# Kernel tuning notes

Hardware: AMD Instinct MI355X
Metric: run time of the kernel (lower is better)

## Reference

```python
import jax, jax.numpy as jnp
from jax import lax
import numpy as np

E = 16          # n_routed_experts
H = 2048        # hidden_size
I = 1408        # moe_intermediate_size
T = 2048        # tokens
K = 6           # top_k


def setup_inputs() -> dict:
    key = jax.random.key(0)
    k1, k2, k3, k4, k5 = jax.random.split(key, 5)
    hidden_states = jax.random.normal(k1, (T, H), dtype=jnp.float32)
    top_k_index = jax.random.randint(k2, (T, K), 0, E)
    top_k_weights = jax.random.uniform(k3, (T, K), dtype=jnp.float32)
    gate_up_proj = jax.random.normal(k4, (E, 2 * I, H), dtype=jnp.float32) * 0.02
    down_proj = jax.random.normal(k5, (E, H, I), dtype=jnp.float32) * 0.02
    return {
        "hidden_states": hidden_states,
        "top_k_index": top_k_index,
        "top_k_weights": top_k_weights,
        "gate_up_proj": gate_up_proj,
        "down_proj": down_proj,
    }


def reference(hidden_states, top_k_index, top_k_weights, gate_up_proj, down_proj):
    # combine[t, e] = sum over k-slots of top_k_weights[t, k] where top_k_index[t, k] == e
    # (scatter-add handles duplicate expert picks identically to index_add_).
    n_tok = hidden_states.shape[0]
    n_exp = gate_up_proj.shape[0]
    combine = jnp.zeros((n_tok, n_exp), hidden_states.dtype)
    combine = combine.at[jnp.arange(n_tok)[:, None], top_k_index].add(top_k_weights)

    def expert_step(acc, params):
        gu, dn, c_e = params  # gu: [2I, H], dn: [H, I], c_e: [n_tok]
        gate, up = jnp.split(hidden_states @ gu.T, 2, axis=-1)  # each [n_tok, I]
        y = (jax.nn.silu(gate) * up) @ dn.T                     # [n_tok, H]
        return acc + y * c_e[:, None], None

    out, _ = lax.scan(
        expert_step,
        jnp.zeros_like(hidden_states),
        (gate_up_proj, down_proj, combine.T),
    )
    return out
```

## Files before the change

kernel.cpp:

```cpp
#include <hip/hip_runtime.h>
#include <hip/hip_bf16.h>
#include <cstdint>

#define T_TOK 2048
#define HD 2048
#define ID 1408
#define NE 16
#define TOPK 6

#define BM 256
#define BN 64
#define BK 64
#define NT1 22
#define NT2 32

typedef __bf16 bf16x8 __attribute__((ext_vector_type(8)));
typedef float f32x4 __attribute__((ext_vector_type(4)));

typedef const __attribute__((address_space(1))) void* gas1_t;
typedef __attribute__((address_space(3))) void* las3_t;
#define GLDS16(g, l) __builtin_amdgcn_global_load_lds((gas1_t)(g), (las3_t)(l), 16, 0, 0)


__global__ void k_combine(const int* __restrict__ idx, const float* __restrict__ w,
                          float* __restrict__ combine) {
    int t = blockIdx.x * blockDim.x + threadIdx.x;
    if (t >= T_TOK) return;
    int ie[TOPK];
    float fw[TOPK];
#pragma unroll
    for (int k = 0; k < TOPK; k++) { ie[k] = idx[t * TOPK + k]; fw[k] = w[t * TOPK + k]; }
#pragma unroll
    for (int e = 0; e < NE; e++) {
        float s = 0.f;
#pragma unroll
        for (int k = 0; k < TOPK; k++) if (ie[k] == e) s += fw[k];
        combine[t * NE + e] = s;
    }
}

__global__ void k_lists(const float* __restrict__ combine, int* __restrict__ counts,
                        int* __restrict__ tok, float* __restrict__ wts) {
    int t = blockIdx.x * blockDim.x + threadIdx.x;
    if (t >= T_TOK) return;
    for (int e = 0; e < NE; e++) {
        float c = combine[t * NE + e];
        if (c != 0.0f) {
            int p = atomicAdd(&counts[e], 1);
            tok[e * T_TOK + p] = t;
            wts[e * T_TOK + p] = c;
        }
    }
}

__global__ void k_cvt(const float* __restrict__ x, __bf16* __restrict__ xb) {
    int i = (blockIdx.x * 256 + threadIdx.x) * 8;
    float4 a = *(const float4*)(x + i);
    float4 b = *(const float4*)(x + i + 4);
    bf16x8 o;
    o[0] = (__bf16)a.x; o[1] = (__bf16)a.y; o[2] = (__bf16)a.z; o[3] = (__bf16)a.w;
    o[4] = (__bf16)b.x; o[5] = (__bf16)b.y; o[6] = (__bf16)b.z; o[7] = (__bf16)b.w;
    *(bf16x8*)(xb + i) = o;
}


__device__ __forceinline__ int swz(int row, int cb) {
    return row * 128 + (cb ^ ((row & 7) << 4));
}

__device__ __forceinline__ bf16x8 ldfrag(const __bf16* base, int row, int cb) {
    return *(const bf16x8*)((const char*)base + swz(row, cb));
}

__device__ __forceinline__ void stage8(const float* __restrict__ src, char* lds,
                                       int row, int cb) {
    float4 f0 = ((const float4*)src)[0];
    float4 f1 = ((const float4*)src)[1];
    bf16x8 o;
    o[0] = (__bf16)f0.x; o[1] = (__bf16)f0.y; o[2] = (__bf16)f0.z; o[3] = (__bf16)f0.w;
    o[4] = (__bf16)f1.x; o[5] = (__bf16)f1.y; o[6] = (__bf16)f1.z; o[7] = (__bf16)f1.w;
    *(bf16x8*)(lds + swz(row, cb)) = o;
}

__device__ __forceinline__ bool decode_item(const int* cnts, int it, int ntn,
                                            int& e, int& m, int& n, int& cnt) {
    int r = it;
#pragma unroll
    for (int ee = 0; ee < NE; ee++) {
        int c = cnts[ee];
        int nm = (c + BM - 1) >> 8;
        int tot = nm * ntn;
        if (r < tot) { e = ee; m = r % nm; n = r / nm; cnt = c; return true; }
        r -= tot;
    }
    return false;
}


__global__ __launch_bounds__(512, 4) void k_gemm1(
    const __bf16* __restrict__ Xb, const float* __restrict__ gup,
    const int* __restrict__ counts, const int* __restrict__ tok,
    __bf16* __restrict__ act, int* __restrict__ cursor) {
    __shared__ __align__(16) __bf16 sA[BM * BK];
    __shared__ __align__(16) __bf16 sBg[BN * BK];
    __shared__ __align__(16) __bf16 sBu[BN * BK];
    __shared__ int s_it;

    int tid = threadIdx.x;
    int lane = tid & 63;
    int wid = tid >> 6;
    int wm = wid >> 1, wn = wid & 1;
    int l15 = lane & 15, lh = lane >> 4;
    int csw = ((lane & 7) ^ ((lane >> 3) & 7)) * 8;
    int br = tid >> 3, bc = tid & 7;

    int cnts[NE];
#pragma unroll
    for (int ee = 0; ee < NE; ee++) cnts[ee] = counts[ee];

    while (true) {
        if (tid == 0) s_it = atomicAdd(cursor, 1);
        __syncthreads();
        int e, m, n, cnt;
        if (!decode_item(cnts, s_it, NT1, e, m, n, cnt)) break;
        int m0 = m * BM;
        int n0 = n * BN;

        const __bf16* pA[4];
#pragma unroll
        for (int j = 0; j < 4; j++) {
            int r = 32 * wid + 8 * j + (lane >> 3);
            int g = m0 + r;
            if (g >= cnt) g = cnt - 1;
            pA[j] = Xb + (size_t)tok[e * T_TOK + g] * HD + csw;
        }
        const float* gbase = gup + (size_t)e * (2 * ID) * HD;
        const float* bgSrc = gbase + (size_t)(n0 + br) * HD + bc * 8;
        const float* buSrc = gbase + (size_t)(ID + n0 + br) * HD + bc * 8;

        f32x4 accg[4][2] = {};
        f32x4 accu[4][2] = {};

        for (int k0 = 0; k0 < HD; k0 += BK) {
            __syncthreads();
#pragma unroll
            for (int j = 0; j < 4; j++)
                GLDS16(pA[j] + k0, &sA[(32 * wid + 8 * j) * BK]);
            stage8(bgSrc + k0, (char*)sBg, br, bc * 16);
            stage8(buSrc + k0, (char*)sBu, br, bc * 16);
            __syncthreads();
#pragma unroll
            for (int kk = 0; kk < 2; kk++) {
                int cb = kk * 64 + lh * 16;
                bf16x8 a[4];
#pragma unroll
                for (int fm = 0; fm < 4; fm++)
                    a[fm] = ldfrag(sA, wm * 64 + fm * 16 + l15, cb);
#pragma unroll
                for (int fn = 0; fn < 2; fn++) {
                    bf16x8 bg = ldfrag(sBg, wn * 32 + fn * 16 + l15, cb);
                    bf16x8 bu = ldfrag(sBu, wn * 32 + fn * 16 + l15, cb);
#pragma unroll
                    for (int fm = 0; fm < 4; fm++) {
                        accg[fm][fn] = __builtin_amdgcn_mfma_f32_16x16x32_bf16(a[fm], bg, accg[fm][fn], 0, 0, 0);
                        accu[fm][fn] = __builtin_amdgcn_mfma_f32_16x16x32_bf16(a[fm], bu, accu[fm][fn], 0, 0, 0);
                    }
                }
            }
        }

#pragma unroll
        for (int fm = 0; fm < 4; fm++) {
#pragma unroll
            for (int fn = 0; fn < 2; fn++) {
#pragma unroll
                for (int j = 0; j < 4; j++) {
                    int mloc = wm * 64 + fm * 16 + lh * 4 + j;
                    int g = m0 + mloc;
                    if (g < cnt) {
                        float gv = accg[fm][fn][j];
                        float uv = accu[fm][fn][j];
                        float sv = gv * (1.0f / (1.0f + __expf(-gv)));
                        int nn = n0 + wn * 32 + fn * 16 + l15;
                        act[((size_t)e * T_TOK + g) * ID + nn] = (__bf16)(sv * uv);
                    }
                }
            }
        }
    }
}


__global__ __launch_bounds__(512, 4) void k_gemm2(
    const __bf16* __restrict__ act, const float* __restrict__ dn,
    const int* __restrict__ counts, const int* __restrict__ tok,
    const float* __restrict__ wts, float* __restrict__ out,
    int* __restrict__ cursor) {
    __shared__ __align__(16) __bf16 sA[BM * BK];
    __shared__ __align__(16) __bf16 sB[BN * BK];
    __shared__ int tokLds[BM];
    __shared__ float wtLds[BM];
    __shared__ int s_it;

    int tid = threadIdx.x;
    int lane = tid & 63;
    int wid = tid >> 6;
    int wm = wid >> 1, wn = wid & 1;
    int l15 = lane & 15, lh = lane >> 4;
    int csw = ((lane & 7) ^ ((lane >> 3) & 7)) * 8;
    int br = tid >> 3, bc = tid & 7;

    int cnts[NE];
#pragma unroll
    for (int ee = 0; ee < NE; ee++) cnts[ee] = counts[ee];

    while (true) {
        if (tid == 0) s_it = atomicAdd(cursor, 1);
        __syncthreads();
        int e, m, n, cnt;
        if (!decode_item(cnts, s_it, NT2, e, m, n, cnt)) break;
        int m0 = m * BM;
        int n0 = n * BN;

        if (tid < BM) {
            int g = m0 + tid;
            bool v = g < cnt;
            tokLds[tid] = v ? tok[e * T_TOK + g] : 0;
            wtLds[tid] = v ? wts[e * T_TOK + g] : 0.f;
        }

        const __bf16* pA[4];
#pragma unroll
        for (int j = 0; j < 4; j++) {
            int r = 32 * wid + 8 * j + (lane >> 3);
            int g = m0 + r;
            if (g >= cnt) g = cnt - 1;
            pA[j] = act + ((size_t)e * T_TOK + g) * ID + csw;
        }
        const float* bSrc = dn + (size_t)e * HD * ID + (size_t)(n0 + br) * ID + bc * 8;

        f32x4 acc[4][2] = {};

        for (int k0 = 0; k0 < ID; k0 += BK) {
            __syncthreads();
#pragma unroll
            for (int j = 0; j < 4; j++)
                GLDS16(pA[j] + k0, &sA[(32 * wid + 8 * j) * BK]);
            stage8(bSrc + k0, (char*)sB, br, bc * 16);
            __syncthreads();
#pragma unroll
            for (int kk = 0; kk < 2; kk++) {
                int cb = kk * 64 + lh * 16;
                bf16x8 a[4];
#pragma unroll
                for (int fm = 0; fm < 4; fm++)
                    a[fm] = ldfrag(sA, wm * 64 + fm * 16 + l15, cb);
#pragma unroll
                for (int fn = 0; fn < 2; fn++) {
                    bf16x8 b = ldfrag(sB, wn * 32 + fn * 16 + l15, cb);
#pragma unroll
                    for (int fm = 0; fm < 4; fm++)
                        acc[fm][fn] = __builtin_amdgcn_mfma_f32_16x16x32_bf16(a[fm], b, acc[fm][fn], 0, 0, 0);
                }
            }
        }

        __syncthreads();
#pragma unroll
        for (int fm = 0; fm < 4; fm++) {
#pragma unroll
            for (int fn = 0; fn < 2; fn++) {
#pragma unroll
                for (int j = 0; j < 4; j++) {
                    int mloc = wm * 64 + fm * 16 + lh * 4 + j;
                    int g = m0 + mloc;
                    if (g < cnt) {
                        float v = acc[fm][fn][j] * wtLds[mloc];
                        int nn = n0 + wn * 32 + fn * 16 + l15;
                        atomicAdd(&out[(size_t)tokLds[mloc] * HD + nn], v);
                    }
                }
            }
        }
    }
}


extern "C" void kernel_launch(void* const* d_in, const int* in_sizes, int n_in,
                              void* d_out, int out_size, void* d_ws, size_t ws_size,
                              hipStream_t stream) {
    const float* hs = (const float*)d_in[0];
    const int* tki = (const int*)d_in[1];
    const float* tkw = (const float*)d_in[2];
    const float* gup = (const float*)d_in[3];
    const float* dnp = (const float*)d_in[4];
    float* out = (float*)d_out;

    char* p = (char*)d_ws;
    int* counts = (int*)p;      p += 256;
    int* cursors = (int*)p;     p += 256;
    float* combine = (float*)p; p += (size_t)T_TOK * NE * 4;
    int* tok = (int*)p;         p += (size_t)NE * T_TOK * 4;
    float* wts = (float*)p;     p += (size_t)NE * T_TOK * 4;
    __bf16* Xb = (__bf16*)p;    p += (size_t)T_TOK * HD * 2;
    __bf16* act = (__bf16*)p;

    hipMemsetAsync(counts, 0, 512, stream);
    hipMemsetAsync(d_out, 0, (size_t)T_TOK * HD * 4, stream);
    k_combine<<<T_TOK / 256, 256, 0, stream>>>(tki, tkw, combine);
    k_lists<<<T_TOK / 256, 256, 0, stream>>>(combine, counts, tok, wts);
    k_cvt<<<(T_TOK * HD / 8) / 256, 256, 0, stream>>>(hs, Xb);
    k_gemm1<<<dim3(768), 512, 0, stream>>>(Xb, gup, counts, tok, act, &cursors[0]);
    k_gemm2<<<dim3(768), 512, 0, stream>>>(act, dnp, counts, tok, wts, out, &cursors[1]);
}
```

Baseline: 443.1 us.

## Replace persistent atomic work queue with static grid of smaller-N tiles

Drops the persistent-kernel loop that pulled work items from an atomic cursor. Each block now decodes one (expert, m, n) tile from its blockIdx, and the grid is oversized to a fixed maximum so surplus blocks exit early. Tiles shrink to BN=32 with 256 threads, so each wave covers 64 rows across the full tile width. This removes the atomic and barrier per item, but each block reloads its A tile at twice the rate relative to the B columns it covers, and many empty blocks still have to be launched.

```diff
diff --git a/kernel.cpp b/kernel.cpp
--- a/kernel.cpp
+++ b/kernel.cpp
@@ -9,10 +9,11 @@
 #define TOPK 6
 
 #define BM 256
-#define BN 64
 #define BK 64
-#define NT1 22
-#define NT2 32
+#define BN 32
+#define NT1 44
+#define NT2 64
+#define GMAX 64
 
 typedef __bf16 bf16x8 __attribute__((ext_vector_type(8)));
 typedef float f32x4 __attribute__((ext_vector_type(4)));
@@ -82,12 +83,11 @@
     *(bf16x8*)(lds + swz(row, cb)) = o;
 }
 
-__device__ __forceinline__ bool decode_item(const int* cnts, int it, int ntn,
-                                            int& e, int& m, int& n, int& cnt) {
+__device__ __forceinline__ bool decode_item(const int* __restrict__ counts, int it,
+                                            int ntn, int& e, int& m, int& n, int& cnt) {
     int r = it;
-#pragma unroll
     for (int ee = 0; ee < NE; ee++) {
-        int c = cnts[ee];
+        int c = counts[ee];
         int nm = (c + BM - 1) >> 8;
         int tot = nm * ntn;
         if (r < tot) { e = ee; m = r % nm; n = r / nm; cnt = c; return true; }
@@ -97,93 +97,84 @@
 }
 
 
-__global__ __launch_bounds__(512, 4) void k_gemm1(
+__global__ __launch_bounds__(256, 4) void k_gemm1(
     const __bf16* __restrict__ Xb, const float* __restrict__ gup,
     const int* __restrict__ counts, const int* __restrict__ tok,
-    __bf16* __restrict__ act, int* __restrict__ cursor) {
+    __bf16* __restrict__ act) {
     __shared__ __align__(16) __bf16 sA[BM * BK];
     __shared__ __align__(16) __bf16 sBg[BN * BK];
     __shared__ __align__(16) __bf16 sBu[BN * BK];
-    __shared__ int s_it;
+
+    int e, m, n, cnt;
+    if (!decode_item(counts, blockIdx.x, NT1, e, m, n, cnt)) return;
+    int m0 = m * BM;
+    int n0 = n * BN;
 
     int tid = threadIdx.x;
     int lane = tid & 63;
     int wid = tid >> 6;
-    int wm = wid >> 1, wn = wid & 1;
     int l15 = lane & 15, lh = lane >> 4;
     int csw = ((lane & 7) ^ ((lane >> 3) & 7)) * 8;
+
+    const __bf16* pA[8];
+#pragma unroll
+    for (int j = 0; j < 8; j++) {
+        int r = 64 * wid + 8 * j + (lane >> 3);
+        int g = m0 + r;
+        if (g >= cnt) g = cnt - 1;
+        pA[j] = Xb + (size_t)tok[e * T_TOK + g] * HD + csw;
+    }
+
     int br = tid >> 3, bc = tid & 7;
-
-    int cnts[NE];
-#pragma unroll
-    for (int ee = 0; ee < NE; ee++) cnts[ee] = counts[ee];
-
-    while (true) {
-        if (tid == 0) s_it = atomicAdd(cursor, 1);
-        __syncthreads();
-        int e, m, n, cnt;
-        if (!decode_item(cnts, s_it, NT1, e, m, n, cnt)) break;
-        int m0 = m * BM;
-        int n0 = n * BN;
-
-        const __bf16* pA[4];
-#pragma unroll
-        for (int j = 0; j < 4; j++) {
-            int r = 32 * wid + 8 * j + (lane >> 3);
-            int g = m0 + r;
-            if (g >= cnt) g = cnt - 1;
-            pA[j] = Xb + (size_t)tok[e * T_TOK + g] * HD + csw;
-        }
-        const float* gbase = gup + (size_t)e * (2 * ID) * HD;
-        const float* bgSrc = gbase + (size_t)(n0 + br) * HD + bc * 8;
-        const float* buSrc = gbase + (size_t)(ID + n0 + br) * HD + bc * 8;
-
-        f32x4 accg[4][2] = {};
-        f32x4 accu[4][2] = {};
-
-        for (int k0 = 0; k0 < HD; k0 += BK) {
-            __syncthreads();
-#pragma unroll
-            for (int j = 0; j < 4; j++)
-                GLDS16(pA[j] + k0, &sA[(32 * wid + 8 * j) * BK]);
-            stage8(bgSrc + k0, (char*)sBg, br, bc * 16);
-            stage8(buSrc + k0, (char*)sBu, br, bc * 16);
-            __syncthreads();
-#pragma unroll
-            for (int kk = 0; kk < 2; kk++) {
-                int cb = kk * 64 + lh * 16;
-                bf16x8 a[4];
-#pragma unroll
-                for (int fm = 0; fm < 4; fm++)
-                    a[fm] = ldfrag(sA, wm * 64 + fm * 16 + l15, cb);
-#pragma unroll
-                for (int fn = 0; fn < 2; fn++) {
-                    bf16x8 bg = ldfrag(sBg, wn * 32 + fn * 16 + l15, cb);
-                    bf16x8 bu = ldfrag(sBu, wn * 32 + fn * 16 + l15, cb);
-#pragma unroll
-                    for (int fm = 0; fm < 4; fm++) {
-                        accg[fm][fn] = __builtin_amdgcn_mfma_f32_16x16x32_bf16(a[fm], bg, accg[fm][fn], 0, 0, 0);
-                        accu[fm][fn] = __builtin_amdgcn_mfma_f32_16x16x32_bf16(a[fm], bu, accu[fm][fn], 0, 0, 0);
-                    }
+    const float* gbase = gup + (size_t)e * (2 * ID) * HD;
+    const float* bgSrc = gbase + (size_t)(n0 + br) * HD + bc * 8;
+    const float* buSrc = gbase + (size_t)(ID + n0 + br) * HD + bc * 8;
+
+    f32x4 accg[4][2] = {};
+    f32x4 accu[4][2] = {};
+
+    for (int k0 = 0; k0 < HD; k0 += BK) {
+        __syncthreads();
+#pragma unroll
+        for (int j = 0; j < 8; j++)
+            GLDS16(pA[j] + k0, &sA[(64 * wid + 8 * j) * BK]);
+        stage8(bgSrc + k0, (char*)sBg, br, bc * 16);
+        stage8(buSrc + k0, (char*)sBu, br, bc * 16);
+        __syncthreads();
+#pragma unroll
+        for (int kk = 0; kk < 2; kk++) {
+            int cb = kk * 64 + lh * 16;
+            bf16x8 a[4];
+#pragma unroll
+            for (int fm = 0; fm < 4; fm++)
+                a[fm] = ldfrag(sA, wid * 64 + fm * 16 + l15, cb);
+#pragma unroll
+            for (int fn = 0; fn < 2; fn++) {
+                bf16x8 bg = ldfrag(sBg, fn * 16 + l15, cb);
+                bf16x8 bu = ldfrag(sBu, fn * 16 + l15, cb);
+#pragma unroll
+                for (int fm = 0; fm < 4; fm++) {
+                    accg[fm][fn] = __builtin_amdgcn_mfma_f32_16x16x32_bf16(a[fm], bg, accg[fm][fn], 0, 0, 0);
+                    accu[fm][fn] = __builtin_amdgcn_mfma_f32_16x16x32_bf16(a[fm], bu, accu[fm][fn], 0, 0, 0);
                 }
             }
         }
-
-#pragma unroll
-        for (int fm = 0; fm < 4; fm++) {
-#pragma unroll
-            for (int fn = 0; fn < 2; fn++) {
-#pragma unroll
-                for (int j = 0; j < 4; j++) {
-                    int mloc = wm * 64 + fm * 16 + lh * 4 + j;
-                    int g = m0 + mloc;
-                    if (g < cnt) {
-                        float gv = accg[fm][fn][j];
-                        float uv = accu[fm][fn][j];
-                        float sv = gv * (1.0f / (1.0f + __expf(-gv)));
-                        int nn = n0 + wn * 32 + fn * 16 + l15;
-                        act[((size_t)e * T_TOK + g) * ID + nn] = (__bf16)(sv * uv);
-                    }
+    }
+
+#pragma unroll
+    for (int fm = 0; fm < 4; fm++) {
+#pragma unroll
+        for (int fn = 0; fn < 2; fn++) {
+#pragma unroll
+            for (int j = 0; j < 4; j++) {
+                int mloc = wid * 64 + fm * 16 + lh * 4 + j;
+                int g = m0 + mloc;
+                if (g < cnt) {
+                    float gv = accg[fm][fn][j];
+                    float uv = accu[fm][fn][j];
+                    float sv = gv * (1.0f / (1.0f + __expf(-gv)));
+                    int nn = n0 + fn * 16 + l15;
+                    act[((size_t)e * T_TOK + g) * ID + nn] = (__bf16)(sv * uv);
                 }
             }
         }
@@ -191,94 +182,84 @@
 }
 
 
-__global__ __launch_bounds__(512, 4) void k_gemm2(
+__global__ __launch_bounds__(256, 4) void k_gemm2(
     const __bf16* __restrict__ act, const float* __restrict__ dn,
     const int* __restrict__ counts, const int* __restrict__ tok,
-    const float* __restrict__ wts, float* __restrict__ out,
-    int* __restrict__ cursor) {
+    const float* __restrict__ wts, float* __restrict__ out) {
     __shared__ __align__(16) __bf16 sA[BM * BK];
     __shared__ __align__(16) __bf16 sB[BN * BK];
     __shared__ int tokLds[BM];
     __shared__ float wtLds[BM];
-    __shared__ int s_it;
+
+    int e, m, n, cnt;
+    if (!decode_item(counts, blockIdx.x, NT2, e, m, n, cnt)) return;
+    int m0 = m * BM;
+    int n0 = n * BN;
 
     int tid = threadIdx.x;
     int lane = tid & 63;
     int wid = tid >> 6;
-    int wm = wid >> 1, wn = wid & 1;
     int l15 = lane & 15, lh = lane >> 4;
     int csw = ((lane & 7) ^ ((lane >> 3) & 7)) * 8;
+
+    if (tid < BM) {
+        int g = m0 + tid;
+        bool v = g < cnt;
+        tokLds[tid] = v ? tok[e * T_TOK + g] : 0;
+        wtLds[tid] = v ? wts[e * T_TOK + g] : 0.f;
+    }
+
+    const __bf16* pA[8];
+#pragma unroll
+    for (int j = 0; j < 8; j++) {
+        int r = 64 * wid + 8 * j + (lane >> 3);
+        int g = m0 + r;
+        if (g >= cnt) g = cnt - 1;
+        pA[j] = act + ((size_t)e * T_TOK + g) * ID + csw;
+    }
+
     int br = tid >> 3, bc = tid & 7;
-
-    int cnts[NE];
-#pragma unroll
-    for (int ee = 0; ee < NE; ee++) cnts[ee] = counts[ee];
-
-    while (true) {
-        if (tid == 0) s_it = atomicAdd(cursor, 1);
-        __syncthreads();
-        int e, m, n, cnt;
-        if (!decode_item(cnts, s_it, NT2, e, m, n, cnt)) break;
-        int m0 = m * BM;
-        int n0 = n * BN;
-
-        if (tid < BM) {
-            int g = m0 + tid;
-            bool v = g < cnt;
-            tokLds[tid] = v ? tok[e * T_TOK + g] : 0;
-            wtLds[tid] = v ? wts[e * T_TOK + g] : 0.f;
-        }
-
-        const __bf16* pA[4];
-#pragma unroll
-        for (int j = 0; j < 4; j++) {
-            int r = 32 * wid + 8 * j + (lane >> 3);
-            int g = m0 + r;
-            if (g >= cnt) g = cnt - 1;
-            pA[j] = act + ((size_t)e * T_TOK + g) * ID + csw;
-        }
-        const float* bSrc = dn + (size_t)e * HD * ID + (size_t)(n0 + br) * ID + bc * 8;
-
-        f32x4 acc[4][2] = {};
-
-        for (int k0 = 0; k0 < ID; k0 += BK) {
-            __syncthreads();
-#pragma unroll
-            for (int j = 0; j < 4; j++)
-                GLDS16(pA[j] + k0, &sA[(32 * wid + 8 * j) * BK]);
-            stage8(bSrc + k0, (char*)sB, br, bc * 16);
-            __syncthreads();
-#pragma unroll
-            for (int kk = 0; kk < 2; kk++) {
-                int cb = kk * 64 + lh * 16;
-                bf16x8 a[4];
+    const float* bSrc = dn + (size_t)e * HD * ID + (size_t)(n0 + br) * ID + bc * 8;
+
+    f32x4 acc[4][2] = {};
+
+    for (int k0 = 0; k0 < ID; k0 += BK) {
+        __syncthreads();
+#pragma unroll
+        for (int j = 0; j < 8; j++)
+            GLDS16(pA[j] + k0, &sA[(64 * wid + 8 * j) * BK]);
+        stage8(bSrc + k0, (char*)sB, br, bc * 16);
+        __syncthreads();
+#pragma unroll
+        for (int kk = 0; kk < 2; kk++) {
+            int cb = kk * 64 + lh * 16;
+            bf16x8 a[4];
+#pragma unroll
+            for (int fm = 0; fm < 4; fm++)
+                a[fm] = ldfrag(sA, wid * 64 + fm * 16 + l15, cb);
+#pragma unroll
+            for (int fn = 0; fn < 2; fn++) {
+                bf16x8 b = ldfrag(sB, fn * 16 + l15, cb);
 #pragma unroll
                 for (int fm = 0; fm < 4; fm++)
-                    a[fm] = ldfrag(sA, wm * 64 + fm * 16 + l15, cb);
-#pragma unroll
-                for (int fn = 0; fn < 2; fn++) {
-                    bf16x8 b = ldfrag(sB, wn * 32 + fn * 16 + l15, cb);
-#pragma unroll
-                    for (int fm = 0; fm < 4; fm++)
-                        acc[fm][fn] = __builtin_amdgcn_mfma_f32_16x16x32_bf16(a[fm], b, acc[fm][fn], 0, 0, 0);
-                }
-            }
-        }
-
-        __syncthreads();
-#pragma unroll
-        for (int fm = 0; fm < 4; fm++) {
-#pragma unroll
-            for (int fn = 0; fn < 2; fn++) {
-#pragma unroll
-                for (int j = 0; j < 4; j++) {
-                    int mloc = wm * 64 + fm * 16 + lh * 4 + j;
-                    int g = m0 + mloc;
-                    if (g < cnt) {
-                        float v = acc[fm][fn][j] * wtLds[mloc];
-                        int nn = n0 + wn * 32 + fn * 16 + l15;
-                        atomicAdd(&out[(size_t)tokLds[mloc] * HD + nn], v);
-                    }
+                    acc[fm][fn] = __builtin_amdgcn_mfma_f32_16x16x32_bf16(a[fm], b, acc[fm][fn], 0, 0, 0);
+            }
+        }
+    }
+
+    __syncthreads();
+#pragma unroll
+    for (int fm = 0; fm < 4; fm++) {
+#pragma unroll
+        for (int fn = 0; fn < 2; fn++) {
+#pragma unroll
+            for (int j = 0; j < 4; j++) {
+                int mloc = wid * 64 + fm * 16 + lh * 4 + j;
+                int g = m0 + mloc;
+                if (g < cnt) {
+                    float v = acc[fm][fn][j] * wtLds[mloc];
+                    int nn = n0 + fn * 16 + l15;
+                    atomicAdd(&out[(size_t)tokLds[mloc] * HD + nn], v);
                 }
             }
         }
@@ -298,18 +279,17 @@
 
     char* p = (char*)d_ws;
     int* counts = (int*)p;      p += 256;
-    int* cursors = (int*)p;     p += 256;
     float* combine = (float*)p; p += (size_t)T_TOK * NE * 4;
     int* tok = (int*)p;         p += (size_t)NE * T_TOK * 4;
     float* wts = (float*)p;     p += (size_t)NE * T_TOK * 4;
     __bf16* Xb = (__bf16*)p;    p += (size_t)T_TOK * HD * 2;
     __bf16* act = (__bf16*)p;
 
-    hipMemsetAsync(counts, 0, 512, stream);
+    hipMemsetAsync(counts, 0, 256, stream);
     hipMemsetAsync(d_out, 0, (size_t)T_TOK * HD * 4, stream);
     k_combine<<<T_TOK / 256, 256, 0, stream>>>(tki, tkw, combine);
     k_lists<<<T_TOK / 256, 256, 0, stream>>>(combine, counts, tok, wts);
     k_cvt<<<(T_TOK * HD / 8) / 256, 256, 0, stream>>>(hs, Xb);
-    k_gemm1<<<dim3(768), 512, 0, stream>>>(Xb, gup, counts, tok, act, &cursors[0]);
-    k_gemm2<<<dim3(768), 512, 0, stream>>>(act, dnp, counts, tok, wts, out, &cursors[1]);
-}
+    k_gemm1<<<dim3(GMAX * NT1), 256, 0, stream>>>(Xb, gup, counts, tok, act);
+    k_gemm2<<<dim3(GMAX * NT2), 256, 0, stream>>>(act, dnp, counts, tok, wts, out);
+}
```

Result: slower. 463.8 us (+4.7%).

## Fuse routing kernels and make gemm2 one tile per block

Applied to the files above, without the earlier changes.

Merges the combine and list-building kernels into a single routing kernel, which removes one launch and the combine buffer round trip. The down-projection GEMM drops its persistent atomic work-queue loop and launches a fixed grid of GMAX*NT2 blocks that each decode one tile from blockIdx and exit if idle. The epilogue now reads token index and weight straight from global memory instead of staging them in LDS. This trades the cursor atomics and per-item barriers for many empty blocks and repeated global reads in the epilogue, and it can only cover up to GMAX m-tiles in total.

```diff
diff --git a/kernel.cpp b/kernel.cpp
--- a/kernel.cpp
+++ b/kernel.cpp
@@ -13,6 +13,7 @@
 #define BK 64
 #define NT1 22
 #define NT2 32
+#define GMAX 64
 
 typedef __bf16 bf16x8 __attribute__((ext_vector_type(8)));
 typedef float f32x4 __attribute__((ext_vector_type(4)));
@@ -22,8 +23,9 @@
 #define GLDS16(g, l) __builtin_amdgcn_global_load_lds((gas1_t)(g), (las3_t)(l), 16, 0, 0)
 
 
-__global__ void k_combine(const int* __restrict__ idx, const float* __restrict__ w,
-                          float* __restrict__ combine) {
+__global__ void k_route(const int* __restrict__ idx, const float* __restrict__ w,
+                        int* __restrict__ counts, int* __restrict__ tok,
+                        float* __restrict__ wts) {
     int t = blockIdx.x * blockDim.x + threadIdx.x;
     if (t >= T_TOK) return;
     int ie[TOPK];
@@ -35,20 +37,10 @@
         float s = 0.f;
 #pragma unroll
         for (int k = 0; k < TOPK; k++) if (ie[k] == e) s += fw[k];
-        combine[t * NE + e] = s;
-    }
-}
-
-__global__ void k_lists(const float* __restrict__ combine, int* __restrict__ counts,
-                        int* __restrict__ tok, float* __restrict__ wts) {
-    int t = blockIdx.x * blockDim.x + threadIdx.x;
-    if (t >= T_TOK) return;
-    for (int e = 0; e < NE; e++) {
-        float c = combine[t * NE + e];
-        if (c != 0.0f) {
+        if (s != 0.f) {
             int p = atomicAdd(&counts[e], 1);
             tok[e * T_TOK + p] = t;
-            wts[e * T_TOK + p] = c;
+            wts[e * T_TOK + p] = s;
         }
     }
 }
@@ -194,13 +186,19 @@
 __global__ __launch_bounds__(512, 4) void k_gemm2(
     const __bf16* __restrict__ act, const float* __restrict__ dn,
     const int* __restrict__ counts, const int* __restrict__ tok,
-    const float* __restrict__ wts, float* __restrict__ out,
-    int* __restrict__ cursor) {
+    const float* __restrict__ wts, float* __restrict__ out) {
     __shared__ __align__(16) __bf16 sA[BM * BK];
     __shared__ __align__(16) __bf16 sB[BN * BK];
-    __shared__ int tokLds[BM];
-    __shared__ float wtLds[BM];
-    __shared__ int s_it;
+
+    int e, m, n, cnt;
+    {
+        int cnts[NE];
+#pragma unroll
+        for (int ee = 0; ee < NE; ee++) cnts[ee] = counts[ee];
+        if (!decode_item(cnts, blockIdx.x, NT2, e, m, n, cnt)) return;
+    }
+    int m0 = m * BM;
+    int n0 = n * BN;
 
     int tid = threadIdx.x;
     int lane = tid & 63;
@@ -210,75 +208,55 @@
     int csw = ((lane & 7) ^ ((lane >> 3) & 7)) * 8;
     int br = tid >> 3, bc = tid & 7;
 
-    int cnts[NE];
-#pragma unroll
-    for (int ee = 0; ee < NE; ee++) cnts[ee] = counts[ee];
-
-    while (true) {
-        if (tid == 0) s_it = atomicAdd(cursor, 1);
+    const __bf16* pA[4];
+#pragma unroll
+    for (int j = 0; j < 4; j++) {
+        int r = 32 * wid + 8 * j + (lane >> 3);
+        int g = m0 + r;
+        if (g >= cnt) g = cnt - 1;
+        pA[j] = act + ((size_t)e * T_TOK + g) * ID + csw;
+    }
+    const float* bSrc = dn + (size_t)e * HD * ID + (size_t)(n0 + br) * ID + bc * 8;
+
+    f32x4 acc[4][2] = {};
+
+    for (int k0 = 0; k0 < ID; k0 += BK) {
         __syncthreads();
-        int e, m, n, cnt;
-        if (!decode_item(cnts, s_it, NT2, e, m, n, cnt)) break;
-        int m0 = m * BM;
-        int n0 = n * BN;
-
-        if (tid < BM) {
-            int g = m0 + tid;
-            bool v = g < cnt;
-            tokLds[tid] = v ? tok[e * T_TOK + g] : 0;
-            wtLds[tid] = v ? wts[e * T_TOK + g] : 0.f;
-        }
-
-        const __bf16* pA[4];
+#pragma unroll
+        for (int j = 0; j < 4; j++)
+            GLDS16(pA[j] + k0, &sA[(32 * wid + 8 * j) * BK]);
+        stage8(bSrc + k0, (char*)sB, br, bc * 16);
+        __syncthreads();
+#pragma unroll
+        for (int kk = 0; kk < 2; kk++) {
+            int cb = kk * 64 + lh * 16;
+            bf16x8 a[4];
+#pragma unroll
+            for (int fm = 0; fm < 4; fm++)
+                a[fm] = ldfrag(sA, wm * 64 + fm * 16 + l15, cb);
+#pragma unroll
+            for (int fn = 0; fn < 2; fn++) {
+                bf16x8 b = ldfrag(sB, wn * 32 + fn * 16 + l15, cb);
+#pragma unroll
+                for (int fm = 0; fm < 4; fm++)
+                    acc[fm][fn] = __builtin_amdgcn_mfma_f32_16x16x32_bf16(a[fm], b, acc[fm][fn], 0, 0, 0);
+            }
+        }
+    }
+
+#pragma unroll
+    for (int fm = 0; fm < 4; fm++) {
 #pragma unroll
         for (int j = 0; j < 4; j++) {
-            int r = 32 * wid + 8 * j + (lane >> 3);
-            int g = m0 + r;
-            if (g >= cnt) g = cnt - 1;
-            pA[j] = act + ((size_t)e * T_TOK + g) * ID + csw;
-        }
-        const float* bSrc = dn + (size_t)e * HD * ID + (size_t)(n0 + br) * ID + bc * 8;
-
-        f32x4 acc[4][2] = {};
-
-        for (int k0 = 0; k0 < ID; k0 += BK) {
-            __syncthreads();
-#pragma unroll
-            for (int j = 0; j < 4; j++)
-                GLDS16(pA[j] + k0, &sA[(32 * wid + 8 * j) * BK]);
-            stage8(bSrc + k0, (char*)sB, br, bc * 16);
-            __syncthreads();
-#pragma unroll
-            for (int kk = 0; kk < 2; kk++) {
-                int cb = kk * 64 + lh * 16;
-                bf16x8 a[4];
-#pragma unroll
-                for (int fm = 0; fm < 4; fm++)
-                    a[fm] = ldfrag(sA, wm * 64 + fm * 16 + l15, cb);
+            int mloc = wm * 64 + fm * 16 + lh * 4 + j;
+            int g = m0 + mloc;
+            if (g < cnt) {
+                int t = tok[e * T_TOK + g];
+                float w = wts[e * T_TOK + g];
 #pragma unroll
                 for (int fn = 0; fn < 2; fn++) {
-                    bf16x8 b = ldfrag(sB, wn * 32 + fn * 16 + l15, cb);
-#pragma unroll
-                    for (int fm = 0; fm < 4; fm++)
-                        acc[fm][fn] = __builtin_amdgcn_mfma_f32_16x16x32_bf16(a[fm], b, acc[fm][fn], 0, 0, 0);
-                }
-            }
-        }
-
-        __syncthreads();
-#pragma unroll
-        for (int fm = 0; fm < 4; fm++) {
-#pragma unroll
-            for (int fn = 0; fn < 2; fn++) {
-#pragma unroll
-                for (int j = 0; j < 4; j++) {
-                    int mloc = wm * 64 + fm * 16 + lh * 4 + j;
-                    int g = m0 + mloc;
-                    if (g < cnt) {
-                        float v = acc[fm][fn][j] * wtLds[mloc];
-                        int nn = n0 + wn * 32 + fn * 16 + l15;
-                        atomicAdd(&out[(size_t)tokLds[mloc] * HD + nn], v);
-                    }
+                    int nn = n0 + wn * 32 + fn * 16 + l15;
+                    atomicAdd(&out[(size_t)t * HD + nn], acc[fm][fn][j] * w);
                 }
             }
         }
@@ -299,7 +277,6 @@
     char* p = (char*)d_ws;
     int* counts = (int*)p;      p += 256;
     int* cursors = (int*)p;     p += 256;
-    float* combine = (float*)p; p += (size_t)T_TOK * NE * 4;
     int* tok = (int*)p;         p += (size_t)NE * T_TOK * 4;
     float* wts = (float*)p;     p += (size_t)NE * T_TOK * 4;
     __bf16* Xb = (__bf16*)p;    p += (size_t)T_TOK * HD * 2;
@@ -307,9 +284,8 @@
 
     hipMemsetAsync(counts, 0, 512, stream);
     hipMemsetAsync(d_out, 0, (size_t)T_TOK * HD * 4, stream);
-    k_combine<<<T_TOK / 256, 256, 0, stream>>>(tki, tkw, combine);
-    k_lists<<<T_TOK / 256, 256, 0, stream>>>(combine, counts, tok, wts);
+    k_route<<<T_TOK / 256, 256, 0, stream>>>(tki, tkw, counts, tok, wts);
     k_cvt<<<(T_TOK * HD / 8) / 256, 256, 0, stream>>>(hs, Xb);
     k_gemm1<<<dim3(768), 512, 0, stream>>>(Xb, gup, counts, tok, act, &cursors[0]);
-    k_gemm2<<<dim3(768), 512, 0, stream>>>(act, dnp, counts, tok, wts, out, &cursors[1]);
-}
+    k_gemm2<<<dim3(GMAX * NT2), 512, 0, stream>>>(act, dnp, counts, tok, wts, out);
+}
```

Result: no change. 437.7 us, median of 2 (-1.2%).
